# Optimization experiments

Measured on AMD Instinct MI355X. Metric: run time of the kernel, lower is better.

The kernel has to match this reference:

```python
import jax, jax.numpy as jnp
import numpy as np

D_MODEL = 1024
N_HEADS = 16
D_HEAD = 64
INIT_RANGE = 0.02
IGNORE = -100000.0


def setup_inputs() -> dict:
    key = jax.random.key(0)
    ks = jax.random.split(key, 5)
    x = jax.random.normal(ks[0], (2, 2048, D_MODEL), dtype=jnp.float32)
    W_Q = jax.random.normal(ks[1], (N_HEADS, D_MODEL, D_HEAD), dtype=jnp.float32) * INIT_RANGE
    W_K = jax.random.normal(ks[2], (N_HEADS, D_MODEL, D_HEAD), dtype=jnp.float32) * INIT_RANGE
    W_V = jax.random.normal(ks[3], (N_HEADS, D_MODEL, D_HEAD), dtype=jnp.float32) * INIT_RANGE
    W_O = jax.random.normal(ks[4], (N_HEADS, D_HEAD, D_MODEL), dtype=jnp.float32) * INIT_RANGE
    b_Q = jnp.zeros((N_HEADS, D_HEAD), dtype=jnp.float32)
    b_K = jnp.zeros((N_HEADS, D_HEAD), dtype=jnp.float32)
    b_V = jnp.zeros((N_HEADS, D_HEAD), dtype=jnp.float32)
    b_O = jnp.zeros((D_MODEL,), dtype=jnp.float32)
    return {"normalized_resid_pre": x, "W_Q": W_Q, "W_K": W_K, "W_V": W_V,
            "W_O": W_O, "b_Q": b_Q, "b_K": b_K, "b_V": b_V, "b_O": b_O}


def reference(normalized_resid_pre, W_Q, W_K, W_V, W_O, b_Q, b_K, b_V, b_O):
    x = normalized_resid_pre  # [b, s, d_model]
    q = jnp.einsum('bsd,hde->bshe', x, W_Q) + b_Q  # [b, s, h, d_head]
    k = jnp.einsum('bsd,hde->bshe', x, W_K) + b_K
    v = jnp.einsum('bsd,hde->bshe', x, W_V) + b_V
    scores = jnp.einsum('bqhe,bkhe->bhqk', q, k) / jnp.sqrt(jnp.float32(D_HEAD))
    s = x.shape[1]
    causal = jnp.arange(s)[:, None] >= jnp.arange(s)[None, :]  # [q, k]
    scores = jnp.where(causal, scores, jnp.float32(IGNORE))
    pattern = jax.nn.softmax(scores, axis=-1)  # [b, h, q, k]
    z = jnp.einsum('bkhe,bhqk->bqhe', v, pattern)
    out = jnp.einsum('bqhe,hed->bqd', z, W_O) + b_O
    return out
```

## Files before the change

kernel.cpp:

```cpp
#include <hip/hip_runtime.h>

#define SEQ 2048
#define BATCH 2
#define DM 1024
#define NH 16
#define DH 64

typedef __bf16 bf16;
typedef __bf16 bf16x8 __attribute__((ext_vector_type(8)));
typedef __bf16 bf16x4 __attribute__((ext_vector_type(4)));
typedef float f32x4 __attribute__((ext_vector_type(4)));

#define MFMA16(a, b, c) __builtin_amdgcn_mfma_f32_16x16x32_bf16((a), (b), (c), 0, 0, 0)

#if __has_builtin(__builtin_amdgcn_exp2f)
#define EXP2(x) __builtin_amdgcn_exp2f(x)
#else
#define EXP2(x) exp2f(x)
#endif

#define QSCALE 0.18033688f

typedef __attribute__((address_space(3))) void lds_void;
typedef __attribute__((address_space(1))) void glb_void;
__device__ __forceinline__ void gld16(void* lds, const void* g) {
    __builtin_amdgcn_global_load_lds((const glb_void*)g, (lds_void*)lds, 16, 0, 0);
}

__global__ __launch_bounds__(256) void k_prep(const float* __restrict__ x,
                                              const float* __restrict__ WQ,
                                              const float* __restrict__ WK,
                                              const float* __restrict__ WV,
                                              const float* __restrict__ WO,
                                              bf16* __restrict__ xb,
                                              bf16* __restrict__ wT,
                                              bf16* __restrict__ woT) {
    int bx = blockIdx.x;
    int t = threadIdx.x;
    if (bx < 2048) {
        int g = bx * 256 + t;
        const float4* x4 = (const float4*)x;
        float4 a = x4[2 * g];
        float4 b = x4[2 * g + 1];
        bf16x8 o;
        o[0] = (bf16)a.x; o[1] = (bf16)a.y; o[2] = (bf16)a.z; o[3] = (bf16)a.w;
        o[4] = (bf16)b.x; o[5] = (bf16)b.y; o[6] = (bf16)b.z; o[7] = (bf16)b.w;
        *(bf16x8*)(xb + 8 * g) = o;
        return;
    }
    __shared__ bf16 T[64 * 65];
    if (bx < 2816) {
        int id = bx - 2048;
        int kt = id & 15, ph = id >> 4;
        int p = ph >> 4, h = ph & 15;
        const float* Wp = (p == 0) ? WQ : (p == 1) ? WK : WV;
        const float* src = Wp + ((size_t)h * DM + (size_t)kt * 64) * DH;
        for (int i = 0; i < 4; i++) {
            int c = t + 256 * i;
            int r = c >> 4;
            int col = (c & 15) * 4;
            float4 v = *(const float4*)&src[r * 64 + col];
            T[(col + 0) * 65 + r] = (bf16)v.x;
            T[(col + 1) * 65 + r] = (bf16)v.y;
            T[(col + 2) * 65 + r] = (bf16)v.z;
            T[(col + 3) * 65 + r] = (bf16)v.w;
        }
        __syncthreads();
        bf16* dst = wT + (size_t)ph * 64 * DM + (size_t)kt * 64;
        for (int i = 0; i < 2; i++) {
            int c = t + 256 * i;
            int e = c >> 3;
            int k0 = (c & 7) * 8;
            bf16x8 o;
            for (int j = 0; j < 8; j++) o[j] = T[e * 65 + k0 + j];
            *(bf16x8*)&dst[(size_t)e * DM + k0] = o;
        }
    } else {
        int id = bx - 2816;
        int ht = id & 15, dt = id >> 4;
        for (int i = 0; i < 4; i++) {
            int c = t + 256 * i;
            int r = c >> 4;
            int col = (c & 15) * 4;
            float4 v = *(const float4*)&WO[((size_t)(ht * 64 + r)) * DM + dt * 64 + col];
            T[(col + 0) * 65 + r] = (bf16)v.x;
            T[(col + 1) * 65 + r] = (bf16)v.y;
            T[(col + 2) * 65 + r] = (bf16)v.z;
            T[(col + 3) * 65 + r] = (bf16)v.w;
        }
        __syncthreads();
        for (int i = 0; i < 2; i++) {
            int c = t + 256 * i;
            int d = c >> 3;
            int h0 = (c & 7) * 8;
            bf16x8 o;
            for (int j = 0; j < 8; j++) o[j] = T[d * 65 + h0 + j];
            *(bf16x8*)&woT[((size_t)(dt * 64 + d)) * DM + ht * 64 + h0] = o;
        }
    }
}

__global__ __launch_bounds__(512, 2) void k_qkv(const bf16* __restrict__ xb,
                                                const bf16* __restrict__ wT,
                                                const float* __restrict__ bQ,
                                                const float* __restrict__ bK,
                                                const float* __restrict__ bV,
                                                bf16* __restrict__ Qb,
                                                bf16* __restrict__ Kb,
                                                bf16* __restrict__ VTf) {
    int mt = blockIdx.x, nt = blockIdx.y, p = blockIdx.z;
    __shared__ __align__(16) char sm[131072];
    int t = threadIdx.x;
    int lane = t & 63, w = t >> 6;
    int l15 = lane & 15, quad = lane >> 4;
    int wr = w >> 2, wc = w & 3;
    int m0 = mt * 256, n0 = nt * 256;

    int P0 = t * 16;
    int L0 = P0 ^ (((P0 >> 7) & 3) << 4);
    int row0 = L0 >> 6, kc0 = (L0 >> 4) & 3;
    int P1 = 8192 + t * 16;
    int L1 = P1 ^ (((P1 >> 7) & 3) << 4);
    int row1 = L1 >> 6, kc1 = (L1 >> 4) & 3;
    const bf16* gA0 = xb + (size_t)(m0 + row0) * DM + kc0 * 8;
    const bf16* gA1 = xb + (size_t)(m0 + row1) * DM + kc1 * 8;
    const bf16* gB0 = wT + (size_t)(p * 1024 + n0 + row0) * DM + kc0 * 8;
    const bf16* gB1 = wT + (size_t)(p * 1024 + n0 + row1) * DM + kc1 * 8;

    auto stage = [&](int ts, bool bsel) {
        char* sb = sm + (ts & 3) * 32768;
        int ko = ts * 32;
        if (!bsel) {
            gld16(sb + w * 1024, gA0 + ko);
            gld16(sb + 8192 + w * 1024, gA1 + ko);
        } else {
            gld16(sb + 16384 + w * 1024, gB0 + ko);
            gld16(sb + 16384 + 8192 + w * 1024, gB1 + ko);
        }
    };

    int aoff[8], boff[4];
#pragma unroll
    for (int mi = 0; mi < 8; mi++) {
        int row = wr * 128 + mi * 16 + l15;
        aoff[mi] = row * 64 + ((quad ^ ((row >> 1) & 3)) << 4);
    }
#pragma unroll
    for (int ni = 0; ni < 4; ni++) {
        int row = wc * 64 + ni * 16 + l15;
        boff[ni] = 16384 + row * 64 + ((quad ^ ((row >> 1) & 3)) << 4);
    }

    const f32x4 z4 = {0.f, 0.f, 0.f, 0.f};
    f32x4 acc[8][4];
#pragma unroll
    for (int mi = 0; mi < 8; mi++)
#pragma unroll
        for (int ni = 0; ni < 4; ni++) acc[mi][ni] = z4;

    auto kstep = [&](int tt, bool st) {
        const char* sb = sm + (tt & 3) * 32768;
        bf16x8 bfr[4], afr[4];
#pragma unroll
        for (int ni = 0; ni < 4; ni++) bfr[ni] = *(const bf16x8*)(sb + boff[ni]);
#pragma unroll
        for (int mi = 0; mi < 4; mi++) afr[mi] = *(const bf16x8*)(sb + aoff[mi]);
        if (st) stage(tt + 3, false);
        __builtin_amdgcn_s_setprio(1);
#pragma unroll
        for (int mi = 0; mi < 4; mi++)
#pragma unroll
            for (int ni = 0; ni < 4; ni++)
                acc[mi][ni] = MFMA16(afr[mi], bfr[ni], acc[mi][ni]);
        __builtin_amdgcn_s_setprio(0);
        asm volatile("s_barrier" ::: "memory");
        bf16x8 afr2[4];
#pragma unroll
        for (int mi = 0; mi < 4; mi++) afr2[mi] = *(const bf16x8*)(sb + aoff[4 + mi]);
        if (st) stage(tt + 3, true);
        __builtin_amdgcn_s_setprio(1);
#pragma unroll
        for (int mi = 0; mi < 4; mi++)
#pragma unroll
            for (int ni = 0; ni < 4; ni++)
                acc[4 + mi][ni] = MFMA16(afr2[mi], bfr[ni], acc[4 + mi][ni]);
        __builtin_amdgcn_s_setprio(0);
    };

    stage(0, false); stage(0, true);
    stage(1, false); stage(1, true);
    stage(2, false); stage(2, true);

#pragma unroll 1
    for (int tt = 0; tt < 29; tt++) {
        asm volatile("s_waitcnt vmcnt(8)\n\ts_barrier" ::: "memory");
        __builtin_amdgcn_sched_barrier(0);
        kstep(tt, true);
    }
    asm volatile("s_waitcnt vmcnt(8)\n\ts_barrier" ::: "memory");
    __builtin_amdgcn_sched_barrier(0);
    kstep(29, false);
    asm volatile("s_waitcnt vmcnt(4)\n\ts_barrier" ::: "memory");
    __builtin_amdgcn_sched_barrier(0);
    kstep(30, false);
    asm volatile("s_waitcnt vmcnt(0)\n\ts_barrier" ::: "memory");
    __builtin_amdgcn_sched_barrier(0);
    kstep(31, false);

    int b = m0 >> 11;
    if (p < 2) {
        const float* bias = (p == 0) ? bQ : bK;
        bf16* dst = (p == 0) ? Qb : Kb;
        float scale = (p == 0) ? QSCALE : 1.0f;
#pragma unroll
        for (int ni = 0; ni < 4; ni++) {
            int he = n0 + wc * 64 + ni * 16 + l15;
            int h = he >> 6, e = he & 63;
            float bia = bias[he];
            size_t rb = (size_t)(b * NH + h) * SEQ * DH + e;
#pragma unroll
            for (int mi = 0; mi < 8; mi++)
#pragma unroll
                for (int r = 0; r < 4; r++) {
                    int s = ((m0 + wr * 128 + mi * 16 + quad * 4 + r) & 2047);
                    dst[rb + (size_t)s * DH] = (bf16)((acc[mi][ni][r] + bia) * scale);
                }
        }
    } else {
#pragma unroll
        for (int ni = 0; ni < 4; ni++) {
            int he = n0 + wc * 64 + ni * 16 + l15;
            int h = he >> 6;
            float bia = bV[he];
#pragma unroll
            for (int mi = 0; mi < 8; mi++) {
                int kvl = (mt & 7) * 256 + wr * 128 + mi * 16;
                int kt = kvl >> 7;
                int f = (mi >> 1) * 4 + ni;
                size_t base = (((size_t)(b * NH + h) * 16 + kt) * 16 + f) * 512
                              + (size_t)((quad << 4) | l15) * 8 + (mi & 1) * 4;
                bf16x4 o;
#pragma unroll
                for (int r = 0; r < 4; r++) o[r] = (bf16)(acc[mi][ni][r] + bia);
                *(bf16x4*)&VTf[base] = o;
            }
        }
    }
}

__global__ __launch_bounds__(512, 4) void k_attn(const bf16* __restrict__ Qb,
                                                 const bf16* __restrict__ Kb,
                                                 const bf16* __restrict__ VTf,
                                                 bf16* __restrict__ Zb) {
    int bh = blockIdx.x;
    int y = blockIdx.y;
    int qt = (y < 8) ? y : 23 - y;
    int h = bh & 15, b = bh >> 4;
    __shared__ __align__(16) bf16 Ks[2][16 * 512];
    __shared__ __align__(16) bf16 Vs[16 * 512];
    int t = threadIdx.x;
    int lane = t & 63, w = t >> 6;
    int l15 = lane & 15, quad = lane >> 4;

    const bf16* qbase = Qb + (size_t)bh * SEQ * DH;
    const bf16* kbase = Kb + (size_t)bh * SEQ * DH;
    const bf16* vfrag = VTf + (size_t)bh * 16 * 8192;

    int qr0 = qt * 128 + w * 16;
    bf16x8 aq[2];
    for (int ks = 0; ks < 2; ks++)
        aq[ks] = *(const bf16x8*)&qbase[(size_t)(qr0 + l15) * DH + ks * 32 + quad * 8];

    auto stageK = [&](int buf, int kt) {
        for (int i = 0; i < 2; i++) {
            int f = w * 2 + i;
            int ks = f >> 3, ni = f & 7;
            gld16(&Ks[buf][f * 512],
                  kbase + (size_t)(kt * 128 + ni * 16 + l15) * DH + ks * 32 + quad * 8);
        }
    };
    auto stageV = [&](int kt) {
        const bf16* vt = vfrag + (size_t)kt * 8192;
        for (int i = 0; i < 2; i++) {
            int f = w * 2 + i;
            gld16(&Vs[f * 512], vt + f * 512 + lane * 8);
        }
    };

    const bf16 one = (bf16)1.0f;
    const bf16x8 ones = {one, one, one, one, one, one, one, one};
    const f32x4 z4 = {0.f, 0.f, 0.f, 0.f};
    f32x4 acco[4], accd;
    for (int no = 0; no < 4; no++) acco[no] = z4;
    accd = z4;

    stageK(0, 0);

    for (int kt = 0; kt <= qt; kt++) {
        int buf = kt & 1;
        __syncthreads();
        stageV(kt);
        if (kt < qt) stageK(buf ^ 1, kt + 1);
        const bf16* Kbuf = Ks[buf];

        f32x4 accs[8];
        for (int ni = 0; ni < 8; ni++) accs[ni] = z4;
        for (int ks = 0; ks < 2; ks++)
            for (int ni = 0; ni < 8; ni++) {
                bf16x8 ak = *(const bf16x8*)&Kbuf[(ks * 8 + ni) * 512 + lane * 8];
                accs[ni] = MFMA16(ak, aq[ks], accs[ni]);
            }

        if (kt == qt) {
            int ql = w * 16 + l15;
            for (int ni = 0; ni < 8; ni++) {
                int kvl = ni * 16 + quad * 4;
                for (int r = 0; r < 4; r++)
                    if (kvl + r > ql) accs[ni][r] = -1e30f;
            }
        }

        bf16x4 pt[8];
        for (int ni = 0; ni < 8; ni++)
            for (int r = 0; r < 4; r++)
                pt[ni][r] = (bf16)EXP2(accs[ni][r]);

        __syncthreads();

        for (int p4 = 0; p4 < 4; p4++) {
            bf16x8 ap;
            for (int j = 0; j < 4; j++) {
                ap[j] = pt[2 * p4][j];
                ap[4 + j] = pt[2 * p4 + 1][j];
            }
            accd = MFMA16(ap, ones, accd);
            for (int no = 0; no < 4; no++) {
                bf16x8 bv = *(const bf16x8*)&Vs[(p4 * 4 + no) * 512 + lane * 8];
                acco[no] = MFMA16(ap, bv, acco[no]);
            }
        }
    }

    for (int r = 0; r < 4; r++) {
        float inv = 1.0f / accd[r];
        int q = qr0 + quad * 4 + r;
        size_t rowbase = ((size_t)b * SEQ + q) * DM + h * DH;
        for (int no = 0; no < 4; no++)
            Zb[rowbase + no * 16 + l15] = (bf16)(acco[no][r] * inv);
    }
}

__global__ __launch_bounds__(256, 4) void k_out(const bf16* __restrict__ Zb,
                                                const bf16* __restrict__ woT,
                                                const float* __restrict__ bO,
                                                float* __restrict__ out) {
    int mt = blockIdx.x;
    int nt = blockIdx.y;
    __shared__ __align__(16) bf16 Ws[2][8 * 512];
    int t = threadIdx.x;
    int lane = t & 63, w = t >> 6;
    int l15 = lane & 15, quad = lane >> 4;

    int m0 = mt * 128, n0 = nt * 64;
    int kl = quad * 8;
    const bf16* a0p = Zb + (size_t)(m0 + w * 32 + l15) * DM + kl;
    const bf16* a1p = a0p + (size_t)16 * DM;
    const bf16* wrow = woT + (size_t)n0 * DM;

    const f32x4 z4 = {0.f, 0.f, 0.f, 0.f};
    f32x4 acc[2][4];
    for (int mi = 0; mi < 2; mi++)
        for (int ni = 0; ni < 4; ni++) acc[mi][ni] = z4;

    auto stageW = [&](int buf, int k0) {
#pragma unroll
        for (int i = 0; i < 2; i++) {
            int f = w * 2 + i;
            int ks = f >> 2, ni = f & 3;
            gld16(&Ws[buf][f * 512],
                  wrow + (size_t)(ni * 16 + l15) * DM + k0 + ks * 32 + quad * 8);
        }
    };

    bf16x8 xr[2][2][2];
    stageW(0, 0);
#pragma unroll
    for (int ks = 0; ks < 2; ks++) {
        xr[0][0][ks] = *(const bf16x8*)(a0p + ks * 32);
        xr[0][1][ks] = *(const bf16x8*)(a1p + ks * 32);
    }

#pragma unroll
    for (int it = 0; it < 16; it++) {
        int buf = it & 1;
        __syncthreads();
        if (it < 15) {
            int kn = (it + 1) * 64;
            stageW(buf ^ 1, kn);
#pragma unroll
            for (int ks = 0; ks < 2; ks++) {
                xr[buf ^ 1][0][ks] = *(const bf16x8*)(a0p + kn + ks * 32);
                xr[buf ^ 1][1][ks] = *(const bf16x8*)(a1p + kn + ks * 32);
            }
        }
#pragma unroll
        for (int ks = 0; ks < 2; ks++) {
#pragma unroll
            for (int ni = 0; ni < 4; ni++) {
                bf16x8 bfr = *(const bf16x8*)&Ws[buf][(ks * 4 + ni) * 512 + lane * 8];
                acc[0][ni] = MFMA16(xr[buf][0][ks], bfr, acc[0][ni]);
                acc[1][ni] = MFMA16(xr[buf][1][ks], bfr, acc[1][ni]);
            }
        }
    }
    for (int ni = 0; ni < 4; ni++) {
        int d = n0 + ni * 16 + l15;
        float bia = bO[d];
        for (int mi = 0; mi < 2; mi++)
            for (int r = 0; r < 4; r++) {
                int s = m0 + w * 32 + mi * 16 + quad * 4 + r;
                out[(size_t)s * DM + d] = acc[mi][ni][r] + bia;
            }
    }
}

extern "C" void kernel_launch(void* const* d_in, const int* in_sizes, int n_in,
                              void* d_out, int out_size, void* d_ws, size_t ws_size,
                              hipStream_t stream) {
    const float* x  = (const float*)d_in[0];
    const float* WQ = (const float*)d_in[1];
    const float* WK = (const float*)d_in[2];
    const float* WV = (const float*)d_in[3];
    const float* WO = (const float*)d_in[4];
    const float* bQ = (const float*)d_in[5];
    const float* bK = (const float*)d_in[6];
    const float* bV = (const float*)d_in[7];
    const float* bO = (const float*)d_in[8];
    float* out = (float*)d_out;

    char* w = (char*)d_ws;
    bf16* xb    = (bf16*)(w + 0);
    bf16* wqkvT = (bf16*)(w + (8u << 20));
    bf16* woT   = (bf16*)(w + (14u << 20));
    bf16* Qb    = (bf16*)(w + (16u << 20));
    bf16* Kb    = (bf16*)(w + (24u << 20));
    bf16* VTf   = (bf16*)(w + (32u << 20));
    bf16* Zb    = (bf16*)(w + (40u << 20));

    k_prep<<<3072, 256, 0, stream>>>(x, WQ, WK, WV, WO, xb, wqkvT, woT);
    k_qkv<<<dim3(16, 4, 3), 512, 0, stream>>>(xb, wqkvT, bQ, bK, bV, Qb, Kb, VTf);
    k_attn<<<dim3(32, 16), 512, 0, stream>>>(Qb, Kb, VTf, Zb);
    k_out<<<dim3(32, 16), 256, 0, stream>>>(Zb, woT, bO, out);
}
```

Measured before the change: 179.1 us.

## Rewrite output GEMM with 4-stage swizzled LDS pipeline and relax barriers

The output projection kernel is restructured to use 128x128 tiles. Both Zb and W_O tiles are staged into a 4-deep XOR-swizzled LDS ring through async global-to-LDS loads, gated by vmcnt-based waits, mirroring the QKV kernel. This is meant to raise data reuse and hide global latency, at the cost of fewer blocks and lower occupancy. The attention loop replaces its __syncthreads with explicit partial vmcnt waits plus s_barrier so K prefetch can stay in flight, and one intra-step barrier in the QKV k-step is removed. That removal may risk an LDS race if the barrier was protecting a buffer being overwritten.

Result: faster. 161.2 us (-10.0%).

```diff
diff --git a/kernel.cpp b/kernel.cpp
--- a/kernel.cpp
+++ b/kernel.cpp
@@ -173,7 +173,6 @@
             for (int ni = 0; ni < 4; ni++)
                 acc[mi][ni] = MFMA16(afr[mi], bfr[ni], acc[mi][ni]);
         __builtin_amdgcn_s_setprio(0);
-        asm volatile("s_barrier" ::: "memory");
         bf16x8 afr2[4];
 #pragma unroll
         for (int mi = 0; mi < 4; mi++) afr2[mi] = *(const bf16x8*)(sb + aoff[4 + mi]);
@@ -298,7 +297,8 @@
 
     for (int kt = 0; kt <= qt; kt++) {
         int buf = kt & 1;
-        __syncthreads();
+        asm volatile("s_waitcnt vmcnt(0)\n\ts_barrier" ::: "memory");
+        __builtin_amdgcn_sched_barrier(0);
         stageV(kt);
         if (kt < qt) stageK(buf ^ 1, kt + 1);
         const bf16* Kbuf = Ks[buf];
@@ -325,7 +325,12 @@
             for (int r = 0; r < 4; r++)
                 pt[ni][r] = (bf16)EXP2(accs[ni][r]);
 
-        __syncthreads();
+        if (kt < qt) {
+            asm volatile("s_waitcnt vmcnt(2)\n\ts_barrier" ::: "memory");
+        } else {
+            asm volatile("s_waitcnt vmcnt(0)\n\ts_barrier" ::: "memory");
+        }
+        __builtin_amdgcn_sched_barrier(0);
 
         for (int p4 = 0; p4 < 4; p4++) {
             bf16x8 ap;
@@ -350,75 +355,101 @@
     }
 }
 
-__global__ __launch_bounds__(256, 4) void k_out(const bf16* __restrict__ Zb,
+__global__ __launch_bounds__(256, 2) void k_out(const bf16* __restrict__ Zb,
                                                 const bf16* __restrict__ woT,
                                                 const float* __restrict__ bO,
                                                 float* __restrict__ out) {
-    int mt = blockIdx.x;
-    int nt = blockIdx.y;
-    __shared__ __align__(16) bf16 Ws[2][8 * 512];
+    int mt = blockIdx.x, nt = blockIdx.y;
+    __shared__ __align__(16) char sm[65536];
     int t = threadIdx.x;
     int lane = t & 63, w = t >> 6;
     int l15 = lane & 15, quad = lane >> 4;
-
-    int m0 = mt * 128, n0 = nt * 64;
-    int kl = quad * 8;
-    const bf16* a0p = Zb + (size_t)(m0 + w * 32 + l15) * DM + kl;
-    const bf16* a1p = a0p + (size_t)16 * DM;
-    const bf16* wrow = woT + (size_t)n0 * DM;
+    int wr = w >> 1, wc = w & 1;
+    int m0 = mt * 128, n0 = nt * 128;
+
+    int P0 = t * 16;
+    int L0 = P0 ^ (((P0 >> 7) & 3) << 4);
+    int row0 = L0 >> 6, kc0 = (L0 >> 4) & 3;
+    int P1 = 4096 + t * 16;
+    int L1 = P1 ^ (((P1 >> 7) & 3) << 4);
+    int row1 = L1 >> 6, kc1 = (L1 >> 4) & 3;
+    const bf16* gA0 = Zb + (size_t)(m0 + row0) * DM + kc0 * 8;
+    const bf16* gA1 = Zb + (size_t)(m0 + row1) * DM + kc1 * 8;
+    const bf16* gB0 = woT + (size_t)(n0 + row0) * DM + kc0 * 8;
+    const bf16* gB1 = woT + (size_t)(n0 + row1) * DM + kc1 * 8;
+
+    auto stage = [&](int ts) {
+        char* sb = sm + (ts & 3) * 16384;
+        int ko = ts * 32;
+        gld16(sb + w * 1024, gA0 + ko);
+        gld16(sb + 4096 + w * 1024, gA1 + ko);
+        gld16(sb + 8192 + w * 1024, gB0 + ko);
+        gld16(sb + 8192 + 4096 + w * 1024, gB1 + ko);
+    };
+
+    int aoff[4], boff[4];
+#pragma unroll
+    for (int mi = 0; mi < 4; mi++) {
+        int row = wr * 64 + mi * 16 + l15;
+        aoff[mi] = row * 64 + ((quad ^ ((row >> 1) & 3)) << 4);
+    }
+#pragma unroll
+    for (int ni = 0; ni < 4; ni++) {
+        int row = wc * 64 + ni * 16 + l15;
+        boff[ni] = 8192 + row * 64 + ((quad ^ ((row >> 1) & 3)) << 4);
+    }
 
     const f32x4 z4 = {0.f, 0.f, 0.f, 0.f};
-    f32x4 acc[2][4];
-    for (int mi = 0; mi < 2; mi++)
+    f32x4 acc[4][4];
+#pragma unroll
+    for (int mi = 0; mi < 4; mi++)
+#pragma unroll
         for (int ni = 0; ni < 4; ni++) acc[mi][ni] = z4;
 
-    auto stageW = [&](int buf, int k0) {
-#pragma unroll
-        for (int i = 0; i < 2; i++) {
-            int f = w * 2 + i;
-            int ks = f >> 2, ni = f & 3;
-            gld16(&Ws[buf][f * 512],
-                  wrow + (size_t)(ni * 16 + l15) * DM + k0 + ks * 32 + quad * 8);
-        }
-    };
-
-    bf16x8 xr[2][2][2];
-    stageW(0, 0);
-#pragma unroll
-    for (int ks = 0; ks < 2; ks++) {
-        xr[0][0][ks] = *(const bf16x8*)(a0p + ks * 32);
-        xr[0][1][ks] = *(const bf16x8*)(a1p + ks * 32);
-    }
-
-#pragma unroll
-    for (int it = 0; it < 16; it++) {
-        int buf = it & 1;
-        __syncthreads();
-        if (it < 15) {
-            int kn = (it + 1) * 64;
-            stageW(buf ^ 1, kn);
-#pragma unroll
-            for (int ks = 0; ks < 2; ks++) {
-                xr[buf ^ 1][0][ks] = *(const bf16x8*)(a0p + kn + ks * 32);
-                xr[buf ^ 1][1][ks] = *(const bf16x8*)(a1p + kn + ks * 32);
-            }
-        }
-#pragma unroll
-        for (int ks = 0; ks < 2; ks++) {
-#pragma unroll
-            for (int ni = 0; ni < 4; ni++) {
-                bf16x8 bfr = *(const bf16x8*)&Ws[buf][(ks * 4 + ni) * 512 + lane * 8];
-                acc[0][ni] = MFMA16(xr[buf][0][ks], bfr, acc[0][ni]);
-                acc[1][ni] = MFMA16(xr[buf][1][ks], bfr, acc[1][ni]);
-            }
-        }
-    }
+    auto kstep = [&](int tt, bool st) {
+        const char* sb = sm + (tt & 3) * 16384;
+        bf16x8 bfr[4], afr[4];
+#pragma unroll
+        for (int ni = 0; ni < 4; ni++) bfr[ni] = *(const bf16x8*)(sb + boff[ni]);
+#pragma unroll
+        for (int mi = 0; mi < 4; mi++) afr[mi] = *(const bf16x8*)(sb + aoff[mi]);
+        if (st) stage(tt + 3);
+        __builtin_amdgcn_s_setprio(1);
+#pragma unroll
+        for (int mi = 0; mi < 4; mi++)
+#pragma unroll
+            for (int ni = 0; ni < 4; ni++)
+                acc[mi][ni] = MFMA16(afr[mi], bfr[ni], acc[mi][ni]);
+        __builtin_amdgcn_s_setprio(0);
+    };
+
+    stage(0); stage(1); stage(2);
+
+#pragma unroll 1
+    for (int tt = 0; tt < 29; tt++) {
+        asm volatile("s_waitcnt vmcnt(8)\n\ts_barrier" ::: "memory");
+        __builtin_amdgcn_sched_barrier(0);
+        kstep(tt, true);
+    }
+    asm volatile("s_waitcnt vmcnt(8)\n\ts_barrier" ::: "memory");
+    __builtin_amdgcn_sched_barrier(0);
+    kstep(29, false);
+    asm volatile("s_waitcnt vmcnt(4)\n\ts_barrier" ::: "memory");
+    __builtin_amdgcn_sched_barrier(0);
+    kstep(30, false);
+    asm volatile("s_waitcnt vmcnt(0)\n\ts_barrier" ::: "memory");
+    __builtin_amdgcn_sched_barrier(0);
+    kstep(31, false);
+
+#pragma unroll
     for (int ni = 0; ni < 4; ni++) {
-        int d = n0 + ni * 16 + l15;
+        int d = n0 + wc * 64 + ni * 16 + l15;
         float bia = bO[d];
-        for (int mi = 0; mi < 2; mi++)
+#pragma unroll
+        for (int mi = 0; mi < 4; mi++)
+#pragma unroll
             for (int r = 0; r < 4; r++) {
-                int s = m0 + w * 32 + mi * 16 + quad * 4 + r;
+                int s = m0 + wr * 64 + mi * 16 + quad * 4 + r;
                 out[(size_t)s * DM + d] = acc[mi][ni][r] + bia;
             }
     }
@@ -450,5 +481,5 @@
     k_prep<<<3072, 256, 0, stream>>>(x, WQ, WK, WV, WO, xb, wqkvT, woT);
     k_qkv<<<dim3(16, 4, 3), 512, 0, stream>>>(xb, wqkvT, bQ, bK, bV, Qb, Kb, VTf);
     k_attn<<<dim3(32, 16), 512, 0, stream>>>(Qb, Kb, VTf, Zb);
-    k_out<<<dim3(32, 16), 256, 0, stream>>>(Zb, woT, bO, out);
-}
+    k_out<<<dim3(32, 8), 256, 0, stream>>>(Zb, woT, bO, out);
+}
```
